# Optimization experiments

Hardware: AMD Instinct MI355X
Metric: run time of the kernel (lower is better)

The kernel has to match this reference:

```python
import jax, jax.numpy as jnp
import numpy as np

B, S, D = 4, 2048, 1024
MULT = 4
INNER = MULT * D
E = 4          # n_expert
K = 1          # top-k
ALPHA = 0.5


def setup_inputs() -> dict:
    key = jax.random.key(0)
    ks = jax.random.split(key, 8)
    std = 0.02
    x = jax.random.normal(ks[0], (B, S, D), jnp.float32)
    W1 = jax.random.normal(ks[1], (D, INNER), jnp.float32) * std
    b1 = jnp.zeros((INNER,), jnp.float32)
    W2 = jax.random.normal(ks[2], (INNER, D), jnp.float32) * std
    b2 = jnp.zeros((D,), jnp.float32)
    Wg = jax.random.normal(ks[3], (D, E), jnp.float32) * std
    ew1 = jax.random.normal(ks[4], (E, D, INNER), jnp.float32) * std
    ew3 = jax.random.normal(ks[5], (E, D, INNER), jnp.float32) * std
    ew2 = jax.random.normal(ks[6], (E, INNER, D), jnp.float32) * std
    return {"x": x, "W1": W1, "b1": b1, "W2": W2, "b2": b2,
            "Wg": Wg, "ew1": ew1, "ew3": ew3, "ew2": ew2}


def reference(x, W1, b1, W2, b2, Wg, ew1, ew3, ew2):
    # Dense branch: Linear -> GELU (exact, torch default) -> Linear
    y_dense = jax.nn.gelu(x @ W1 + b1, approximate=False) @ W2 + b2

    # MoE branch: top-k softmax routing, SwiGLU experts
    logits = x @ Wg                                   # [B,S,E]
    probs = jax.nn.softmax(logits, axis=-1)
    topv, topi = jax.lax.top_k(probs, K)              # [B,S,K]
    gates = topv / jnp.sum(topv, axis=-1, keepdims=True)  # renormalize top-k
    onehot = jax.nn.one_hot(topi, E, dtype=x.dtype)   # [B,S,K,E]
    combine = jnp.sum(gates[..., None] * onehot, axis=-2)  # [B,S,E]

    y_moe = jnp.zeros_like(x)
    for e in range(E):  # small fixed expert count
        h = jax.nn.silu(x @ ew1[e]) * (x @ ew3[e])    # [B,S,INNER]
        y_moe = y_moe + combine[..., e:e + 1] * (h @ ew2[e])

    # Load-balancing aux loss: E * sum_e f_e * P_e
    frac = jnp.mean(jnp.sum(onehot, axis=-2), axis=(0, 1)) / K  # [E]
    pmean = jnp.mean(probs, axis=(0, 1))                        # [E]
    aux = E * jnp.sum(frac * pmean)

    y = ALPHA * y_dense + (1.0 - ALPHA) * y_moe
    return (y, aux)
```

## Files before the change

### kernel.cpp

```cpp
#include <hip/hip_runtime.h>
#include <hip/hip_bf16.h>


static constexpr int MT = 8192;
static constexpr int DD = 1024;
static constexpr int DI = 4096;

typedef float f32x4 __attribute__((ext_vector_type(4)));
typedef __bf16 bf16x8 __attribute__((ext_vector_type(8)));
typedef unsigned short u16;

__device__ __forceinline__ u16 f2bf(float f) {
    union { __hip_bfloat16 b; u16 u; } v;
    v.b = __float2bfloat16(f);
    return v.u;
}

__device__ __forceinline__ void gload_lds16(const void* g, void* l) {
    __builtin_amdgcn_global_load_lds(
        (const __attribute__((address_space(1))) void*)g,
        (__attribute__((address_space(3))) void*)l, 16, 0, 0);
}

__device__ __forceinline__ float gelu_f(float v) {
    return 0.5f * v * (1.0f + erff(v * 0.70710678118654752f));
}
__device__ __forceinline__ float silu_f(float v) {
    return v / (1.0f + expf(-v));
}

#define FENCE() asm volatile("" ::: "memory")
#define BARRIER() do { FENCE(); __builtin_amdgcn_s_barrier(); FENCE(); } while (0)
#define WAIT_LGKM0() asm volatile("s_waitcnt lgkmcnt(0)" ::: "memory")

__device__ __forceinline__ void transpose_tile(
    const float* __restrict__ s, u16* __restrict__ d, int K, int N,
    int pack, int packOff) {
    __shared__ u16 t[64][72];
    int n0 = blockIdx.x * 64, k0 = blockIdx.y * 64;
    int tid = threadIdx.x;
    int c = tid & 15;
    int r = tid >> 4;
#pragma unroll
    for (int p = 0; p < 4; ++p) {
        int k = r + p * 16;
        float4 v = *(const float4*)(s + (size_t)(k0 + k) * N + n0 + c * 4);
        t[c * 4 + 0][k] = f2bf(v.x);
        t[c * 4 + 1][k] = f2bf(v.y);
        t[c * 4 + 2][k] = f2bf(v.z);
        t[c * 4 + 3][k] = f2bf(v.w);
    }
    __syncthreads();
    int n = tid >> 2, kc = (tid & 3) * 16;
    const uint4* p0 = (const uint4*)&t[n][kc];
    uint4 a = p0[0], b = p0[1];
    int gn = n0 + n;
    int dr = pack ? ((gn >> 5) * 64 + (gn & 31) + packOff) : gn;
    uint4* o = (uint4*)(d + (size_t)dr * K + k0 + kc);
    o[0] = a; o[1] = b;
}

__global__ void __launch_bounds__(256) transpose_up(
    const float* __restrict__ W1, const float* __restrict__ ew1,
    const float* __restrict__ ew3, u16* __restrict__ W1t,
    u16* __restrict__ ew13t) {
    int z = blockIdx.z;
    if (z == 0) {
        transpose_tile(W1, W1t, DD, DI, 0, 0);
    } else if (z <= 4) {
        transpose_tile(ew1 + (size_t)(z - 1) * DD * DI,
                       ew13t + (size_t)(z - 1) * 2 * DD * DI, DD, DI, 1, 0);
    } else {
        transpose_tile(ew3 + (size_t)(z - 5) * DD * DI,
                       ew13t + (size_t)(z - 5) * 2 * DD * DI, DD, DI, 1, 32);
    }
}

__global__ void __launch_bounds__(256) transpose_dn(
    const float* __restrict__ W2, const float* __restrict__ ew2,
    u16* __restrict__ W2t, u16* __restrict__ ew2t) {
    int z = blockIdx.z;
    if (z == 0) {
        transpose_tile(W2, W2t, DI, DD, 0, 0);
    } else {
        transpose_tile(ew2 + (size_t)(z - 1) * DI * DD,
                       ew2t + (size_t)(z - 1) * DI * DD, DI, DD, 0, 0);
    }
}

__global__ void __launch_bounds__(256) gate_kernel(
    const float* __restrict__ x, const float* __restrict__ Wg,
    float* __restrict__ psum_blk, int* __restrict__ expertA) {
    int w = threadIdx.x >> 6, l = threadIdx.x & 63;
    int t = blockIdx.x * 4 + w;
    const float* xr = x + (size_t)t * DD;
    double a0 = 0, a1 = 0, a2 = 0, a3 = 0;
#pragma unroll
    for (int i = 0; i < 4; ++i) {
        int k = i * 256 + l * 4;
        float4 xv = *(const float4*)(xr + k);
        float4 w0 = *(const float4*)(Wg + (size_t)(k + 0) * 4);
        float4 w1 = *(const float4*)(Wg + (size_t)(k + 1) * 4);
        float4 w2 = *(const float4*)(Wg + (size_t)(k + 2) * 4);
        float4 w3 = *(const float4*)(Wg + (size_t)(k + 3) * 4);
        a0 += (double)xv.x * w0.x + (double)xv.y * w1.x + (double)xv.z * w2.x + (double)xv.w * w3.x;
        a1 += (double)xv.x * w0.y + (double)xv.y * w1.y + (double)xv.z * w2.y + (double)xv.w * w3.y;
        a2 += (double)xv.x * w0.z + (double)xv.y * w1.z + (double)xv.z * w2.z + (double)xv.w * w3.z;
        a3 += (double)xv.x * w0.w + (double)xv.y * w1.w + (double)xv.z * w2.w + (double)xv.w * w3.w;
    }
#pragma unroll
    for (int o = 32; o; o >>= 1) {
        a0 += __shfl_down(a0, o); a1 += __shfl_down(a1, o);
        a2 += __shfl_down(a2, o); a3 += __shfl_down(a3, o);
    }
    __shared__ float wps[4][4];
    if (l == 0) {
        double lg[4] = {a0, a1, a2, a3};
        int best = 0;
#pragma unroll
        for (int e = 1; e < 4; ++e) if (lg[e] > lg[best]) best = e;
        double m = lg[best], s = 0, p[4];
#pragma unroll
        for (int e = 0; e < 4; ++e) { p[e] = exp(lg[e] - m); s += p[e]; }
#pragma unroll
        for (int e = 0; e < 4; ++e) wps[w][e] = (float)(p[e] / s);
        expertA[t] = best;
    }
    __syncthreads();
    if (threadIdx.x < 4)
        psum_blk[blockIdx.x * 4 + threadIdx.x] =
            wps[0][threadIdx.x] + wps[1][threadIdx.x] + wps[2][threadIdx.x] + wps[3][threadIdx.x];
}

__global__ void __launch_bounds__(1024) build_lists(
    const int* __restrict__ expertA, const float* __restrict__ psum_blk,
    int* __restrict__ dstArr, int* __restrict__ rev,
    int* __restrict__ offsets, float* __restrict__ auxOut) {
    __shared__ int sc[4][1024];
    __shared__ float fs[1024];
    __shared__ float psum_s[4];
    __shared__ int tot_s[4], off_s[4];
    int tid = threadIdx.x;
    int le[8]; int c[4] = {0, 0, 0, 0};
#pragma unroll
    for (int i = 0; i < 8; ++i) { int e = expertA[tid * 8 + i]; le[i] = e; c[e]++; }
#pragma unroll
    for (int e = 0; e < 4; ++e) sc[e][tid] = c[e];
    __syncthreads();
    for (int o = 1; o < 1024; o <<= 1) {
        int v[4];
#pragma unroll
        for (int e = 0; e < 4; ++e) v[e] = (tid >= o) ? sc[e][tid - o] : 0;
        __syncthreads();
#pragma unroll
        for (int e = 0; e < 4; ++e) if (tid >= o) sc[e][tid] += v[e];
        __syncthreads();
    }
    if (tid == 0) {
        int o = 0;
#pragma unroll
        for (int e = 0; e < 4; ++e) {
            tot_s[e] = sc[e][1023]; off_s[e] = o; offsets[e] = o; o += tot_s[e];
        }
        offsets[4] = o;
    }
    __syncthreads();
    int base[4];
#pragma unroll
    for (int e = 0; e < 4; ++e) base[e] = off_s[e] + sc[e][tid] - c[e];
#pragma unroll
    for (int i = 0; i < 8; ++i) {
        int e = le[i]; int d = base[e]++; int t = tid * 8 + i;
        dstArr[t] = d; rev[d] = t;
    }
    float ps[4];
#pragma unroll
    for (int e = 0; e < 4; ++e)
        ps[e] = psum_blk[(2 * tid) * 4 + e] + psum_blk[(2 * tid + 1) * 4 + e];
    for (int e = 0; e < 4; ++e) {
        fs[tid] = ps[e]; __syncthreads();
        for (int o = 512; o; o >>= 1) { if (tid < o) fs[tid] += fs[tid + o]; __syncthreads(); }
        if (tid == 0) psum_s[e] = fs[0];
        __syncthreads();
    }
    if (tid == 0) {
        float a = 0;
#pragma unroll
        for (int e = 0; e < 4; ++e)
            a += ((float)tot_s[e] * (1.f / 8192.f)) * (psum_s[e] * (1.f / 8192.f));
        auxOut[0] = 4.f * a;
    }
}

__global__ void __launch_bounds__(256) gather_kernel(
    const float* __restrict__ x, const int* __restrict__ dstArr,
    u16* __restrict__ xg) {
    int w = threadIdx.x >> 6, l = threadIdx.x & 63;
    int t = blockIdx.x * 4 + w;
    int dst = dstArr[t];
    const float* xr = x + (size_t)t * DD;
#pragma unroll
    for (int i = 0; i < 4; ++i) {
        int k = i * 256 + l * 4;
        float4 v = *(const float4*)(xr + k);
        ushort4 u;
        u.x = f2bf(v.x); u.y = f2bf(v.y); u.z = f2bf(v.z); u.w = f2bf(v.w);
        *(ushort4*)(xg + (size_t)dst * DD + k) = u;
    }
}

template <int MODE, int NF>
__global__ void __launch_bounds__(512, 2) gemm8(
    const u16* __restrict__ A, const u16* __restrict__ Bw,
    const float* __restrict__ bias,
    u16* __restrict__ outB, float* __restrict__ outF,
    const int* __restrict__ offsets, const int* __restrict__ rev,
    int N, int K) {
    constexpr int BN   = NF * 64;
    constexpr int WCW  = NF * 16;
    constexpr int AELT = 2 * 256 * 32;
    constexpr int BUFE = AELT + 2 * BN * 32;
    constexpr int NIB  = NF / 2;
    __shared__ u16 lds[2 * BUFE];

    const int tid = threadIdx.x;
    const int w = tid >> 6, l = tid & 63;
    const int lr = l & 15, lg = l >> 4;
    const int wr = w >> 2, wc = w & 3;

    int rowBase, rowsValid = 256;
    const u16* Bp = Bw;
    if constexpr (MODE >= 2) {
        int e = blockIdx.z;
        int off = offsets[e], cnt = offsets[e + 1] - off;
        if ((int)blockIdx.y * 256 >= cnt) return;
        rowBase = off + blockIdx.y * 256;
        rowsValid = cnt - (int)blockIdx.y * 256;
        if (rowsValid > 256) rowsValid = 256;
        Bp = Bw + (size_t)e * ((size_t)2 * DD * DI);
    } else {
        rowBase = blockIdx.y * 256;
    }
    const int colBase = blockIdx.x * BN;
    const int NT = K >> 6;

    auto stageA = [&](int kt, int b, int ks) {
        const int kk = (kt << 6) + (ks << 5);
#pragma unroll
        for (int i = 0; i < 2; ++i) {
            int o = ((w << 1) + i) * 512 + (l << 3);
            int o2 = o ^ (((o >> 8) & 1) << 4);
            gload_lds16(A + (size_t)(rowBase + (o2 >> 5)) * K + kk + (o2 & 31),
                        &lds[b * BUFE + ks * 8192 + ((w << 1) + i) * 512]);
        }
    };
    auto stageB = [&](int kt, int b, int ks) {
        const int kk = (kt << 6) + (ks << 5);
#pragma unroll
        for (int i = 0; i < NIB; ++i) {
            int o = (w * NIB + i) * 512 + (l << 3);
            int o2 = o ^ (((o >> 8) & 1) << 4);
            gload_lds16(Bp + (size_t)(colBase + (o2 >> 5)) * K + kk + (o2 & 31),
                        &lds[b * BUFE + AELT + ks * (BN * 32) + (w * NIB + i) * 512]);
        }
    };

#define WAIT_VMB() do { \
    if constexpr (NF == 4) asm volatile("s_waitcnt vmcnt(4)" ::: "memory"); \
    else                   asm volatile("s_waitcnt vmcnt(3)" ::: "memory"); \
} while (0)

#define READBF(b_, ks_) do { \
    _Pragma("unroll") \
    for (int n = 0; n < NF; ++n) { \
        int e_ = (wc * WCW + n * 16 + lr) * 32 + lg * 8; \
        e_ ^= ((e_ >> 8) & 1) << 4; \
        bf[n] = *(const bf16x8*)&lds[(b_) * BUFE + AELT + (ks_) * (BN * 32) + e_]; \
    } \
} while (0)

#define READAF(b_, ks_, mq_) do { \
    _Pragma("unroll") \
    for (int m = 0; m < 4; ++m) { \
        int e_ = (wr * 128 + ((mq_) * 4 + m) * 16 + lr) * 32 + lg * 8; \
        e_ ^= ((e_ >> 8) & 1) << 4; \
        af[m] = *(const bf16x8*)&lds[(b_) * BUFE + (ks_) * 8192 + e_]; \
    } \
} while (0)

#define DOMFMA(mq_) do { \
    __builtin_amdgcn_s_setprio(1); \
    _Pragma("unroll") \
    for (int m = 0; m < 4; ++m) \
    _Pragma("unroll") \
    for (int n = 0; n < NF; ++n) \
        acc[(mq_) * 4 + m][n] = __builtin_amdgcn_mfma_f32_16x16x32_bf16( \
            bf[n], af[m], acc[(mq_) * 4 + m][n], 0, 0, 0); \
    __builtin_amdgcn_s_setprio(0); \
} while (0)

    f32x4 acc[8][NF];
#pragma unroll
    for (int m = 0; m < 8; ++m)
#pragma unroll
        for (int n = 0; n < NF; ++n) acc[m][n] = (f32x4){0.f, 0.f, 0.f, 0.f};
    bf16x8 af[4], bf[NF];

    stageA(0, 0, 0); stageB(0, 0, 0); stageA(0, 0, 1); stageB(0, 0, 1);
    stageA(1, 1, 0); stageB(1, 1, 0);
    WAIT_VMB();
    BARRIER();

    for (int t = 0; t < NT; ++t) {
        const int cb = t & 1, nb = cb ^ 1;
        const int tp1 = (t + 1 < NT) ? t + 1 : NT - 1;
        const int tp2 = (t + 2 < NT) ? t + 2 : NT - 1;
        READBF(cb, 0); READAF(cb, 0, 0); stageA(tp1, nb, 1);
        BARRIER(); WAIT_LGKM0(); DOMFMA(0); BARRIER();
        READAF(cb, 0, 1); stageB(tp1, nb, 1);
        BARRIER(); WAIT_LGKM0(); DOMFMA(1); BARRIER();
        READBF(cb, 1); READAF(cb, 1, 0); stageA(tp2, cb, 0);
        BARRIER(); WAIT_LGKM0(); DOMFMA(0); BARRIER();
        READAF(cb, 1, 1); stageB(tp2, cb, 0);
        BARRIER(); WAIT_LGKM0(); DOMFMA(1);
        WAIT_VMB();
        BARRIER();
    }

#pragma unroll
    for (int m = 0; m < 8; ++m) {
        int rloc = wr * 128 + m * 16 + lr;
        if (MODE >= 2 && rloc >= rowsValid) continue;
        size_t grow = (size_t)(rowBase + rloc);
        if constexpr (MODE == 2) {
#pragma unroll
            for (int n = 0; n < 2; ++n) {
                int col = (colBase >> 1) + wc * 32 + n * 16 + lg * 4;
                f32x4 v1 = acc[m][n], v3 = acc[m][n + 2];
                ushort4 u;
                u.x = f2bf(silu_f(v1[0]) * v3[0]);
                u.y = f2bf(silu_f(v1[1]) * v3[1]);
                u.z = f2bf(silu_f(v1[2]) * v3[2]);
                u.w = f2bf(silu_f(v1[3]) * v3[3]);
                *(ushort4*)(outB + grow * N + col) = u;
            }
        } else {
#pragma unroll
            for (int n = 0; n < NF; ++n) {
                int col = colBase + wc * WCW + n * 16 + lg * 4;
                f32x4 v = acc[m][n];
                f32x4 bb = *(const f32x4*)(bias + col);
                ushort4 u;
                u.x = f2bf(gelu_f(v[0] + bb[0]));
                u.y = f2bf(gelu_f(v[1] + bb[1]));
                u.z = f2bf(gelu_f(v[2] + bb[2]));
                u.w = f2bf(gelu_f(v[3] + bb[3]));
                *(ushort4*)(outB + grow * N + col) = u;
            }
        }
    }
#undef WAIT_VMB
#undef READBF
#undef READAF
#undef DOMFMA
}

__global__ void __launch_bounds__(256) gemm97cat(
    const u16* __restrict__ Ad, const u16* __restrict__ Ag,
    const u16* __restrict__ W2t, const u16* __restrict__ ew2t,
    const float* __restrict__ b2, float* __restrict__ y,
    const int* __restrict__ offsets, const int* __restrict__ rev) {
    __shared__ u16 ldsA[128 * 32];
    __shared__ u16 ldsB[128 * 32];
    int tid = threadIdx.x, w = tid >> 6, l = tid & 63;
    int wr = w >> 1, wc = w & 1;

    int wg = blockIdx.x;
    int c = wg & 7;
    int s = wg >> 3;
    int x = s & 7;
    int p = c + ((s >> 3) << 3);
    int e = p >> 6;
    int yl = p & 63;

    int off = offsets[e], cnt = offsets[e + 1] - off;
    if (yl * 128 >= cnt) return;
    int rowBase = off + yl * 128;
    int rowsValid = cnt - yl * 128;
    if (rowsValid > 128) rowsValid = 128;
    int colBase = x * 128;

    f32x4 acc[4][4];
#pragma unroll
    for (int m = 0; m < 4; ++m)
#pragma unroll
        for (int n = 0; n < 4; ++n) acc[m][n] = (f32x4){0.f, 0.f, 0.f, 0.f};

    int lr = l & 15, lg = l >> 4;
    int ar = l >> 2, ac = (l & 3) * 8;

    const u16* Bm = ew2t + (size_t)e * DD * DI;
#pragma unroll 1
    for (int half = 0; half < 2; ++half) {
        const u16* Ap = half ? Ag : Ad;
        const u16* Bp = half ? Bm : W2t;
#pragma unroll 1
        for (int kt = 0; kt < DI / 32; ++kt) {
            int k0 = kt << 5;
            const u16* ga = Ap + (size_t)(rowBase + w * 32 + ar) * DI + k0 + ac;
            gload_lds16(ga, &ldsA[(w * 32) * 32]);
            gload_lds16(ga + (size_t)16 * DI, &ldsA[(w * 32 + 16) * 32]);
            const u16* gb = Bp + (size_t)(colBase + w * 32 + ar) * DI + k0 + ac;
            gload_lds16(gb, &ldsB[(w * 32) * 32]);
            gload_lds16(gb + (size_t)16 * DI, &ldsB[(w * 32 + 16) * 32]);
            __syncthreads();
            bf16x8 af[4], bfr[4];
#pragma unroll
            for (int m = 0; m < 4; ++m)
                af[m] = *(const bf16x8*)&ldsA[(wr * 64 + m * 16 + lr) * 32 + lg * 8];
#pragma unroll
            for (int n = 0; n < 4; ++n)
                bfr[n] = *(const bf16x8*)&ldsB[(wc * 64 + n * 16 + lr) * 32 + lg * 8];
#pragma unroll
            for (int m = 0; m < 4; ++m)
#pragma unroll
                for (int n = 0; n < 4; ++n)
                    acc[m][n] = __builtin_amdgcn_mfma_f32_16x16x32_bf16(
                        bfr[n], af[m], acc[m][n], 0, 0, 0);
            __syncthreads();
        }
    }

#pragma unroll
    for (int m = 0; m < 4; ++m) {
        int rloc = wr * 64 + m * 16 + lr;
        if (rloc >= rowsValid) continue;
        int tok = rev[rowBase + rloc];
#pragma unroll
        for (int n = 0; n < 4; ++n) {
            int col = colBase + wc * 64 + n * 16 + lg * 4;
            f32x4 v = acc[m][n];
            f32x4 bb = *(const f32x4*)(b2 + col);
            f32x4 r;
#pragma unroll
            for (int j = 0; j < 4; ++j) r[j] = 0.5f * (v[j] + bb[j]);
            *(f32x4*)(y + (size_t)tok * DD + col) = r;
        }
    }
}

extern "C" void kernel_launch(void* const* d_in, const int* in_sizes, int n_in,
                              void* d_out, int out_size, void* d_ws, size_t ws_size,
                              hipStream_t stream) {
    const float* x   = (const float*)d_in[0];
    const float* W1  = (const float*)d_in[1];
    const float* b1  = (const float*)d_in[2];
    const float* W2  = (const float*)d_in[3];
    const float* b2  = (const float*)d_in[4];
    const float* Wg  = (const float*)d_in[5];
    const float* ew1 = (const float*)d_in[6];
    const float* ew3 = (const float*)d_in[7];
    const float* ew2 = (const float*)d_in[8];
    float* y = (float*)d_out;
    float* auxOut = y + (size_t)MT * DD;

    char* ws = (char*)d_ws;
    size_t off = 0;
    auto take = [&](size_t b) -> void* {
        void* p = ws + off;
        off += (b + 255) & ~(size_t)255;
        return p;
    };
    u16* W1t   = (u16*)take((size_t)DI * DD * 2);
    u16* W2t   = (u16*)take((size_t)DI * DD * 2);
    u16* ew2t  = (u16*)take((size_t)4 * DI * DD * 2);
    u16* xg    = (u16*)take((size_t)(MT + 256) * DD * 2);
    u16* hg    = (u16*)take((size_t)(MT + 256) * DI * 2);
    int* expertA  = (int*)take(MT * 4);
    int* dstArr   = (int*)take(MT * 4);
    int* revA     = (int*)take(MT * 4);
    float* psum_blk = (float*)take(2048 * 4 * 4);
    int* offsets  = (int*)take(64);
    size_t ew13Bytes = (size_t)4 * 2 * DI * DD * 2;
    size_t hdBytes   = (size_t)(MT + 256) * DI * 2;
    u16* ew13t = (u16*)take(ew13Bytes > hdBytes ? ew13Bytes : hdBytes);
    u16* hd    = ew13t;

    if (ws_size < off) return;

    dim3 blk(256);
    transpose_up<<<dim3(DI / 64, DD / 64, 9), blk, 0, stream>>>(W1, ew1, ew3, W1t, ew13t);
    transpose_dn<<<dim3(DD / 64, DI / 64, 5), blk, 0, stream>>>(W2, ew2, W2t, ew2t);
    gate_kernel<<<2048, 256, 0, stream>>>(x, Wg, psum_blk, expertA);
    build_lists<<<1, 1024, 0, stream>>>(expertA, psum_blk, dstArr, revA, offsets, auxOut);
    gather_kernel<<<2048, 256, 0, stream>>>(x, dstArr, xg);
    gemm8<2, 4><<<dim3(2 * DI / 256, MT / 256, 4), dim3(512), 0, stream>>>(
        xg, ew13t, nullptr, hg, nullptr, offsets, nullptr, DI, DD);
    gemm8<0, 4><<<dim3(DI / 256, MT / 256), dim3(512), 0, stream>>>(
        xg, W1t, b1, hd, nullptr, nullptr, nullptr, DI, DD);
    gemm97cat<<<dim3(2048), blk, 0, stream>>>(
        hd, hg, W2t, ew2t, b2, y, offsets, revA);
}
```

Before: 573.4 us.

## Double-buffer LDS tiles in concatenated down-projection GEMM with swizzled layout

Converts the combined dense+expert down-projection GEMM from a single-buffered loop into a two-stage LDS double buffer that prefetches tile kt+2 while computing tile kt, and merges the two K halves into one flat loop. It also XOR-swizzles the LDS layout to reduce bank conflicts on fragment reads. The goal is to hide global load latency behind MFMA work. In exchange it doubles LDS use, which may lower occupancy, and it depends on the new vmcnt waits being correct.

```diff
diff --git a/kernel.cpp b/kernel.cpp
--- a/kernel.cpp
+++ b/kernel.cpp
@@ -370,8 +370,8 @@
     const u16* __restrict__ W2t, const u16* __restrict__ ew2t,
     const float* __restrict__ b2, float* __restrict__ y,
     const int* __restrict__ offsets, const int* __restrict__ rev) {
-    __shared__ u16 ldsA[128 * 32];
-    __shared__ u16 ldsB[128 * 32];
+    __shared__ u16 ldsA[2][128 * 32];
+    __shared__ u16 ldsB[2][128 * 32];
     int tid = threadIdx.x, w = tid >> 6, l = tid & 63;
     int wr = w >> 1, wc = w & 1;
 
@@ -397,38 +397,60 @@
         for (int n = 0; n < 4; ++n) acc[m][n] = (f32x4){0.f, 0.f, 0.f, 0.f};
 
     int lr = l & 15, lg = l >> 4;
-    int ar = l >> 2, ac = (l & 3) * 8;
-
     const u16* Bm = ew2t + (size_t)e * DD * DI;
-#pragma unroll 1
-    for (int half = 0; half < 2; ++half) {
+    constexpr int NT = 2 * DI / 32;
+
+    auto stage = [&](int kt, int b) {
+        int half = kt >> 7;
+        const int k0 = (kt & 127) << 5;
         const u16* Ap = half ? Ag : Ad;
         const u16* Bp = half ? Bm : W2t;
-#pragma unroll 1
-        for (int kt = 0; kt < DI / 32; ++kt) {
-            int k0 = kt << 5;
-            const u16* ga = Ap + (size_t)(rowBase + w * 32 + ar) * DI + k0 + ac;
-            gload_lds16(ga, &ldsA[(w * 32) * 32]);
-            gload_lds16(ga + (size_t)16 * DI, &ldsA[(w * 32 + 16) * 32]);
-            const u16* gb = Bp + (size_t)(colBase + w * 32 + ar) * DI + k0 + ac;
-            gload_lds16(gb, &ldsB[(w * 32) * 32]);
-            gload_lds16(gb + (size_t)16 * DI, &ldsB[(w * 32 + 16) * 32]);
-            __syncthreads();
-            bf16x8 af[4], bfr[4];
-#pragma unroll
-            for (int m = 0; m < 4; ++m)
-                af[m] = *(const bf16x8*)&ldsA[(wr * 64 + m * 16 + lr) * 32 + lg * 8];
+#pragma unroll
+        for (int i = 0; i < 2; ++i) {
+            int o = (w * 2 + i) * 512 + (l << 3);
+            int o2 = o ^ (((o >> 8) & 1) << 4);
+            gload_lds16(Ap + (size_t)(rowBase + (o2 >> 5)) * DI + k0 + (o2 & 31),
+                        &ldsA[b][(w * 2 + i) * 512]);
+            gload_lds16(Bp + (size_t)(colBase + (o2 >> 5)) * DI + k0 + (o2 & 31),
+                        &ldsB[b][(w * 2 + i) * 512]);
+        }
+    };
+
+    stage(0, 0);
+    stage(1, 1);
+    asm volatile("s_waitcnt vmcnt(4)" ::: "memory");
+    BARRIER();
+
+    for (int kt = 0; kt < NT; ++kt) {
+        const int cb = kt & 1;
+        bf16x8 af[4], bfr[4];
+#pragma unroll
+        for (int m = 0; m < 4; ++m) {
+            int e_ = (wr * 64 + m * 16 + lr) * 32 + lg * 8;
+            e_ ^= ((e_ >> 8) & 1) << 4;
+            af[m] = *(const bf16x8*)&ldsA[cb][e_];
+        }
+#pragma unroll
+        for (int n = 0; n < 4; ++n) {
+            int e_ = (wc * 64 + n * 16 + lr) * 32 + lg * 8;
+            e_ ^= ((e_ >> 8) & 1) << 4;
+            bfr[n] = *(const bf16x8*)&ldsB[cb][e_];
+        }
+        WAIT_LGKM0();
+#pragma unroll
+        for (int m = 0; m < 4; ++m)
 #pragma unroll
             for (int n = 0; n < 4; ++n)
-                bfr[n] = *(const bf16x8*)&ldsB[(wc * 64 + n * 16 + lr) * 32 + lg * 8];
-#pragma unroll
-            for (int m = 0; m < 4; ++m)
-#pragma unroll
-                for (int n = 0; n < 4; ++n)
-                    acc[m][n] = __builtin_amdgcn_mfma_f32_16x16x32_bf16(
-                        bfr[n], af[m], acc[m][n], 0, 0, 0);
-            __syncthreads();
-        }
+                acc[m][n] = __builtin_amdgcn_mfma_f32_16x16x32_bf16(
+                    bfr[n], af[m], acc[m][n], 0, 0, 0);
+        BARRIER();
+        if (kt + 2 < NT) {
+            stage(kt + 2, cb);
+            asm volatile("s_waitcnt vmcnt(4)" ::: "memory");
+        } else {
+            asm volatile("s_waitcnt vmcnt(0)" ::: "memory");
+        }
+        BARRIER();
     }
 
 #pragma unroll
```

Measured after the change: 597.9 us. 1.04x slower.

## Split dense and expert down-projection K halves into separate blocks with atomic accumulation

Applied to the files above, without the earlier changes.

The final down-projection GEMM used to run each output tile as one block looping over both the dense and expert K ranges. Now the dense and expert halves are separate workgroups (64 dense row tiles plus up to 256 expert tiles), each doing half the K loop, and they combine results into y with float atomicAdd after the output is zeroed by a memset. This halves per-block serial work and improves load balance across CUs. In exchange it adds a full-output memset, scalar fp32 atomics on every output element, and nondeterministic summation order.

```diff
diff --git a/kernel.cpp b/kernel.cpp
--- a/kernel.cpp
+++ b/kernel.cpp
@@ -365,7 +365,7 @@
 #undef DOMFMA
 }
 
-__global__ void __launch_bounds__(256) gemm97cat(
+__global__ void __launch_bounds__(256) gemm97sk(
     const u16* __restrict__ Ad, const u16* __restrict__ Ag,
     const u16* __restrict__ W2t, const u16* __restrict__ ew2t,
     const float* __restrict__ b2, float* __restrict__ y,
@@ -380,14 +380,24 @@
     int s = wg >> 3;
     int x = s & 7;
     int p = c + ((s >> 3) << 3);
-    int e = p >> 6;
-    int yl = p & 63;
-
-    int off = offsets[e], cnt = offsets[e + 1] - off;
-    if (yl * 128 >= cnt) return;
-    int rowBase = off + yl * 128;
-    int rowsValid = cnt - yl * 128;
-    if (rowsValid > 128) rowsValid = 128;
+
+    const u16* Ap;
+    const u16* Bp;
+    int rowBase, rowsValid = 128;
+    bool dense = (p < 64);
+    if (dense) {
+        rowBase = p * 128;
+        Ap = Ad; Bp = W2t;
+    } else {
+        int pm = p - 64;
+        int e = pm >> 6, yl = pm & 63;
+        int off = offsets[e], cnt = offsets[e + 1] - off;
+        if (yl * 128 >= cnt) return;
+        rowBase = off + yl * 128;
+        rowsValid = cnt - yl * 128;
+        if (rowsValid > 128) rowsValid = 128;
+        Ap = Ag; Bp = ew2t + (size_t)e * DD * DI;
+    }
     int colBase = x * 128;
 
     f32x4 acc[4][4];
@@ -399,36 +409,30 @@
     int lr = l & 15, lg = l >> 4;
     int ar = l >> 2, ac = (l & 3) * 8;
 
-    const u16* Bm = ew2t + (size_t)e * DD * DI;
 #pragma unroll 1
-    for (int half = 0; half < 2; ++half) {
-        const u16* Ap = half ? Ag : Ad;
-        const u16* Bp = half ? Bm : W2t;
-#pragma unroll 1
-        for (int kt = 0; kt < DI / 32; ++kt) {
-            int k0 = kt << 5;
-            const u16* ga = Ap + (size_t)(rowBase + w * 32 + ar) * DI + k0 + ac;
-            gload_lds16(ga, &ldsA[(w * 32) * 32]);
-            gload_lds16(ga + (size_t)16 * DI, &ldsA[(w * 32 + 16) * 32]);
-            const u16* gb = Bp + (size_t)(colBase + w * 32 + ar) * DI + k0 + ac;
-            gload_lds16(gb, &ldsB[(w * 32) * 32]);
-            gload_lds16(gb + (size_t)16 * DI, &ldsB[(w * 32 + 16) * 32]);
-            __syncthreads();
-            bf16x8 af[4], bfr[4];
-#pragma unroll
-            for (int m = 0; m < 4; ++m)
-                af[m] = *(const bf16x8*)&ldsA[(wr * 64 + m * 16 + lr) * 32 + lg * 8];
+    for (int kt = 0; kt < DI / 32; ++kt) {
+        int k0 = kt << 5;
+        const u16* ga = Ap + (size_t)(rowBase + w * 32 + ar) * DI + k0 + ac;
+        gload_lds16(ga, &ldsA[(w * 32) * 32]);
+        gload_lds16(ga + (size_t)16 * DI, &ldsA[(w * 32 + 16) * 32]);
+        const u16* gb = Bp + (size_t)(colBase + w * 32 + ar) * DI + k0 + ac;
+        gload_lds16(gb, &ldsB[(w * 32) * 32]);
+        gload_lds16(gb + (size_t)16 * DI, &ldsB[(w * 32 + 16) * 32]);
+        __syncthreads();
+        bf16x8 af[4], bfr[4];
+#pragma unroll
+        for (int m = 0; m < 4; ++m)
+            af[m] = *(const bf16x8*)&ldsA[(wr * 64 + m * 16 + lr) * 32 + lg * 8];
+#pragma unroll
+        for (int n = 0; n < 4; ++n)
+            bfr[n] = *(const bf16x8*)&ldsB[(wc * 64 + n * 16 + lr) * 32 + lg * 8];
+#pragma unroll
+        for (int m = 0; m < 4; ++m)
 #pragma unroll
             for (int n = 0; n < 4; ++n)
-                bfr[n] = *(const bf16x8*)&ldsB[(wc * 64 + n * 16 + lr) * 32 + lg * 8];
-#pragma unroll
-            for (int m = 0; m < 4; ++m)
-#pragma unroll
-                for (int n = 0; n < 4; ++n)
-                    acc[m][n] = __builtin_amdgcn_mfma_f32_16x16x32_bf16(
-                        bfr[n], af[m], acc[m][n], 0, 0, 0);
-            __syncthreads();
-        }
+                acc[m][n] = __builtin_amdgcn_mfma_f32_16x16x32_bf16(
+                    bfr[n], af[m], acc[m][n], 0, 0, 0);
+        __syncthreads();
     }
 
 #pragma unroll
@@ -436,15 +440,21 @@
         int rloc = wr * 64 + m * 16 + lr;
         if (rloc >= rowsValid) continue;
         int tok = rev[rowBase + rloc];
+        float* yr = y + (size_t)tok * DD;
 #pragma unroll
         for (int n = 0; n < 4; ++n) {
             int col = colBase + wc * 64 + n * 16 + lg * 4;
             f32x4 v = acc[m][n];
-            f32x4 bb = *(const f32x4*)(b2 + col);
-            f32x4 r;
-#pragma unroll
-            for (int j = 0; j < 4; ++j) r[j] = 0.5f * (v[j] + bb[j]);
-            *(f32x4*)(y + (size_t)tok * DD + col) = r;
+            if (dense) {
+                f32x4 bb = *(const f32x4*)(b2 + col);
+#pragma unroll
+                for (int j = 0; j < 4; ++j)
+                    atomicAdd(yr + col + j, 0.5f * (v[j] + bb[j]));
+            } else {
+#pragma unroll
+                for (int j = 0; j < 4; ++j)
+                    atomicAdd(yr + col + j, 0.5f * v[j]);
+            }
         }
     }
 }
@@ -489,6 +499,7 @@
     if (ws_size < off) return;
 
     dim3 blk(256);
+    hipMemsetAsync(y, 0, (size_t)MT * DD * sizeof(float), stream);
     transpose_up<<<dim3(DI / 64, DD / 64, 9), blk, 0, stream>>>(W1, ew1, ew3, W1t, ew13t);
     transpose_dn<<<dim3(DD / 64, DI / 64, 5), blk, 0, stream>>>(W2, ew2, W2t, ew2t);
     gate_kernel<<<2048, 256, 0, stream>>>(x, Wg, psum_blk, expertA);
@@ -498,6 +509,6 @@
         xg, ew13t, nullptr, hg, nullptr, offsets, nullptr, DI, DD);
     gemm8<0, 4><<<dim3(DI / 256, MT / 256), dim3(512), 0, stream>>>(
         xg, W1t, b1, hd, nullptr, nullptr, nullptr, DI, DD);
-    gemm97cat<<<dim3(2048), blk, 0, stream>>>(
+    gemm97sk<<<dim3(2560), blk, 0, stream>>>(
         hd, hg, W2t, ew2t, b2, y, offsets, revA);
 }
```

Measured after the change: 773.6 us. 1.35x slower.

## Double-buffer LDS tiles in second GEMM to overlap global loads with MFMA

Applied to the files above, without the earlier changes.

The concatenated down-projection GEMM now keeps two LDS buffers for the A and B tiles. It issues the global-to-LDS loads for the next K tile before running MFMAs on the current one, which hides load latency behind compute and cuts one barrier per iteration. The two K halves are merged into a single loop, and s_setprio wraps the MFMA block. This doubles LDS use, which may lower occupancy. The correctness of waiting for async global_load_lds with only __syncthreads and no explicit vmcnt wait depends on the compiler inserting that wait.

```diff
diff --git a/kernel.cpp b/kernel.cpp
--- a/kernel.cpp
+++ b/kernel.cpp
@@ -370,8 +370,8 @@
     const u16* __restrict__ W2t, const u16* __restrict__ ew2t,
     const float* __restrict__ b2, float* __restrict__ y,
     const int* __restrict__ offsets, const int* __restrict__ rev) {
-    __shared__ u16 ldsA[128 * 32];
-    __shared__ u16 ldsB[128 * 32];
+    __shared__ u16 ldsA[2][128 * 32];
+    __shared__ u16 ldsB[2][128 * 32];
     int tid = threadIdx.x, w = tid >> 6, l = tid & 63;
     int wr = w >> 1, wc = w & 1;
 
@@ -398,37 +398,45 @@
 
     int lr = l & 15, lg = l >> 4;
     int ar = l >> 2, ac = (l & 3) * 8;
-
     const u16* Bm = ew2t + (size_t)e * DD * DI;
-#pragma unroll 1
-    for (int half = 0; half < 2; ++half) {
+    constexpr int NT = 2 * DI / 32;
+
+    auto stage = [&](int kt, int b) {
+        int half = kt >> 7;
+        int k0 = (kt & 127) << 5;
         const u16* Ap = half ? Ag : Ad;
         const u16* Bp = half ? Bm : W2t;
+        const u16* ga = Ap + (size_t)(rowBase + w * 32 + ar) * DI + k0 + ac;
+        gload_lds16(ga, &ldsA[b][(w * 32) * 32]);
+        gload_lds16(ga + (size_t)16 * DI, &ldsA[b][(w * 32 + 16) * 32]);
+        const u16* gb = Bp + (size_t)(colBase + w * 32 + ar) * DI + k0 + ac;
+        gload_lds16(gb, &ldsB[b][(w * 32) * 32]);
+        gload_lds16(gb + (size_t)16 * DI, &ldsB[b][(w * 32 + 16) * 32]);
+    };
+
+    stage(0, 0);
+    __syncthreads();
+
 #pragma unroll 1
-        for (int kt = 0; kt < DI / 32; ++kt) {
-            int k0 = kt << 5;
-            const u16* ga = Ap + (size_t)(rowBase + w * 32 + ar) * DI + k0 + ac;
-            gload_lds16(ga, &ldsA[(w * 32) * 32]);
-            gload_lds16(ga + (size_t)16 * DI, &ldsA[(w * 32 + 16) * 32]);
-            const u16* gb = Bp + (size_t)(colBase + w * 32 + ar) * DI + k0 + ac;
-            gload_lds16(gb, &ldsB[(w * 32) * 32]);
-            gload_lds16(gb + (size_t)16 * DI, &ldsB[(w * 32 + 16) * 32]);
-            __syncthreads();
-            bf16x8 af[4], bfr[4];
-#pragma unroll
-            for (int m = 0; m < 4; ++m)
-                af[m] = *(const bf16x8*)&ldsA[(wr * 64 + m * 16 + lr) * 32 + lg * 8];
+    for (int kt = 0; kt < NT; ++kt) {
+        const int cb = kt & 1;
+        if (kt + 1 < NT) stage(kt + 1, cb ^ 1);
+        bf16x8 af[4], bfr[4];
+#pragma unroll
+        for (int m = 0; m < 4; ++m)
+            af[m] = *(const bf16x8*)&ldsA[cb][(wr * 64 + m * 16 + lr) * 32 + lg * 8];
+#pragma unroll
+        for (int n = 0; n < 4; ++n)
+            bfr[n] = *(const bf16x8*)&ldsB[cb][(wc * 64 + n * 16 + lr) * 32 + lg * 8];
+        __builtin_amdgcn_s_setprio(1);
+#pragma unroll
+        for (int m = 0; m < 4; ++m)
 #pragma unroll
             for (int n = 0; n < 4; ++n)
-                bfr[n] = *(const bf16x8*)&ldsB[(wc * 64 + n * 16 + lr) * 32 + lg * 8];
-#pragma unroll
-            for (int m = 0; m < 4; ++m)
-#pragma unroll
-                for (int n = 0; n < 4; ++n)
-                    acc[m][n] = __builtin_amdgcn_mfma_f32_16x16x32_bf16(
-                        bfr[n], af[m], acc[m][n], 0, 0, 0);
-            __syncthreads();
-        }
+                acc[m][n] = __builtin_amdgcn_mfma_f32_16x16x32_bf16(
+                    bfr[n], af[m], acc[m][n], 0, 0, 0);
+        __builtin_amdgcn_s_setprio(0);
+        __syncthreads();
     }
 
 #pragma unroll
```

Result: no change. 570.4 us, median of 2 (-0.5%).
